# Optimization experiments

Hardware: AMD Instinct MI355X
Metric: run time of the kernel (lower is better)

Reference implementation:

```python
import jax, jax.numpy as jnp
import numpy as np

PC_RANGE = [-51.2, -51.2, -5.0, 51.2, 51.2, 3.0]
VOXEL = [0.1, 0.1, 0.2]
OSF = 8
NUM_PRIOR = 100
C = 256
BN_EPS = 1e-5
LN_EPS = 1e-5


def _conv(x, w, pad):
    # x: [B,C,H,W], w: [O,I,kh,kw]
    return jax.lax.conv_general_dilated(
        x, w, window_strides=(1, 1), padding=[(pad, pad), (pad, pad)],
        dimension_numbers=('NCHW', 'OIHW', 'NCHW'))


def _bn(x, g, b, m, v):
    scale = (g / jnp.sqrt(v + BN_EPS))[None, :, None, None]
    return (x - m[None, :, None, None]) * scale + b[None, :, None, None]


def setup_inputs() -> dict:
    key = jax.random.key(0)
    ks = jax.random.split(key, 24)
    s3 = 1.0 / np.sqrt(C * 9)
    s1 = 1.0 / np.sqrt(C)
    inp = {
        'bev_feat': jax.random.normal(ks[0], (4, C, 128, 128), jnp.float32),
        'template_anchor': jax.random.normal(ks[1], (4, 900, 11), jnp.float32),
        # shared_conv: 3x3 conv (no bias) + BN(eval) + ReLU
        'shared_w': jax.random.normal(ks[2], (C, C, 3, 3), jnp.float32) * s3,
        'bn1_g': jax.random.normal(ks[3], (C,), jnp.float32) * 0.1 + 1.0,
        'bn1_b': jax.random.normal(ks[4], (C,), jnp.float32) * 0.1,
        'bn1_m': jax.random.normal(ks[5], (C,), jnp.float32) * 0.1,
        'bn1_v': jax.random.uniform(ks[6], (C,), jnp.float32) + 0.5,
        # objectness: 3x3 conv (no bias) + BN + ReLU + 1x1 conv (bias=-2)
        'obj_w1': jax.random.normal(ks[7], (C, C, 3, 3), jnp.float32) * s3,
        'bn2_g': jax.random.normal(ks[8], (C,), jnp.float32) * 0.1 + 1.0,
        'bn2_b': jax.random.normal(ks[9], (C,), jnp.float32) * 0.1,
        'bn2_m': jax.random.normal(ks[10], (C,), jnp.float32) * 0.1,
        'bn2_v': jax.random.uniform(ks[11], (C,), jnp.float32) + 0.5,
        'obj_w2': jax.random.normal(ks[12], (1, C, 1, 1), jnp.float32) * s1,
        'obj_b2': jnp.full((1,), -2.0, jnp.float32),
        # feat_proj: Linear + LN + ReLU + Linear
        'fp_w1': jax.random.normal(ks[13], (C, C), jnp.float32) * s1,
        'fp_b1': jax.random.normal(ks[14], (C,), jnp.float32) * 0.01,
        'ln_g': jnp.ones((C,), jnp.float32),
        'ln_b': jnp.zeros((C,), jnp.float32),
        'fp_w2': jax.random.normal(ks[15], (C, C), jnp.float32) * s1,
        'fp_b2': jax.random.normal(ks[16], (C,), jnp.float32) * 0.01,
        # geometry heads (1x1 convs, bias init 0)
        'z_w': jax.random.normal(ks[17], (1, C, 1, 1), jnp.float32) * s1,
        'z_b': jnp.zeros((1,), jnp.float32),
        'dim_w': jax.random.normal(ks[18], (3, C, 1, 1), jnp.float32) * s1,
        'dim_b': jnp.zeros((3,), jnp.float32),
        'yaw_w': jax.random.normal(ks[19], (2, C, 1, 1), jnp.float32) * s1,
        'yaw_b': jnp.zeros((2,), jnp.float32),
        'vel_w': jax.random.normal(ks[20], (2, C, 1, 1), jnp.float32) * s1,
        'vel_b': jnp.zeros((2,), jnp.float32),
    }
    return inp


def _forward(bev_feat, template_anchor, shared_w, bn1_g, bn1_b, bn1_m, bn1_v,
             obj_w1, bn2_g, bn2_b, bn2_m, bn2_v, obj_w2, obj_b2,
             fp_w1, fp_b1, ln_g, ln_b, fp_w2, fp_b2,
             z_w, z_b, dim_w, dim_b, yaw_w, yaw_b, vel_w, vel_b):
    B, Cc, H, W = bev_feat.shape
    # shared_conv
    feat = jax.nn.relu(_bn(_conv(bev_feat, shared_w, 1), bn1_g, bn1_b, bn1_m, bn1_v))
    # objectness heatmap
    h = jax.nn.relu(_bn(_conv(feat, obj_w1, 1), bn2_g, bn2_b, bn2_m, bn2_v))
    heatmap = jax.nn.sigmoid(_conv(h, obj_w2, 0) + obj_b2[None, :, None, None])
    score = heatmap.reshape(B, H * W)
    K = min(NUM_PRIOR, H * W, template_anchor.shape[1])
    topk_score, topk_inds = jax.lax.top_k(score, K)  # [B,K]
    ys = topk_inds // W
    xs = topk_inds % W
    # gather BEV features at topk locations: [B,K,C]
    feat_flat = feat.reshape(B, Cc, H * W).transpose(0, 2, 1)
    gathered = jnp.take_along_axis(feat_flat, topk_inds[:, :, None], axis=1)
    # feat_proj: Linear + LN + ReLU + Linear
    x = gathered @ fp_w1.T + fp_b1
    mu = jnp.mean(x, axis=-1, keepdims=True)
    var = jnp.mean((x - mu) ** 2, axis=-1, keepdims=True)
    x = (x - mu) / jnp.sqrt(var + LN_EPS) * ln_g + ln_b
    x = jax.nn.relu(x)
    prior_feature = x @ fp_w2.T + fp_b2
    prior_feature = prior_feature * (1.0 + topk_score[:, :, None])
    # geometry heads (1x1 convs == linear on gathered features)
    z_pred = gathered @ z_w[:, :, 0, 0].T + z_b      # [B,K,1]
    dim_pred = gathered @ dim_w[:, :, 0, 0].T + dim_b  # [B,K,3]
    yaw_pred = gathered @ yaw_w[:, :, 0, 0].T + yaw_b  # [B,K,2]
    vel_pred = gathered @ vel_w[:, :, 0, 0].T + vel_b  # [B,K,2]
    # anchor update
    pa = template_anchor[:, :K, :]
    x_metric = (xs.astype(pa.dtype) + 0.5) * (VOXEL[0] * OSF) + PC_RANGE[0]
    y_metric = (ys.astype(pa.dtype) + 0.5) * (VOXEL[1] * OSF) + PC_RANGE[1]
    z_new = pa[..., 2] + 0.5 * z_pred[..., 0]
    dims_new = pa[..., 3:6] + 0.2 * jnp.clip(dim_pred, -1.0, 1.0)
    yaw = jnp.tanh(yaw_pred)
    nrm = jnp.maximum(jnp.sqrt(jnp.sum(yaw * yaw, axis=-1, keepdims=True)), 1e-6)
    yaw_new = 0.7 * pa[..., 6:8] + 0.3 * (yaw / nrm)
    vel_new = pa[..., 8:10] + 0.2 * jnp.clip(vel_pred, -2.0, 2.0)
    prior_anchor = jnp.concatenate([
        x_metric[..., None], y_metric[..., None], z_new[..., None],
        dims_new, yaw_new, vel_new, pa[..., 10:]], axis=-1)
    return prior_feature, prior_anchor, topk_score


def reference(bev_feat, template_anchor, shared_w, bn1_g, bn1_b, bn1_m, bn1_v,
              obj_w1, bn2_g, bn2_b, bn2_m, bn2_v, obj_w2, obj_b2,
              fp_w1, fp_b1, ln_g, ln_b, fp_w2, fp_b2,
              z_w, z_b, dim_w, dim_b, yaw_w, yaw_b, vel_w, vel_b):
    return _forward(bev_feat, template_anchor, shared_w, bn1_g, bn1_b, bn1_m, bn1_v,
                    obj_w1, bn2_g, bn2_b, bn2_m, bn2_v, obj_w2, obj_b2,
                    fp_w1, fp_b1, ln_g, ln_b, fp_w2, fp_b2,
                    z_w, z_b, dim_w, dim_b, yaw_w, yaw_b, vel_w, vel_b)
```

## Files before the change

### kernel.cpp

```cpp
#include <hip/hip_runtime.h>
#include <math.h>


typedef __attribute__((ext_vector_type(8))) short bf16x8;
typedef __attribute__((ext_vector_type(4))) float f32x4;

#define HW 16384
#define WPITCH 130
#define CCAP 192
#define PSTR 28
#define WSO_XN    0ULL
#define WSO_FEATB 34078720ULL
#define WSO_WP1   68157440ULL
#define WSO_WP2   69337088ULL
#define WSO_BNP   70516736ULL
#define WSO_LOG   70521856ULL
#define WSO_CAND  70784000ULL
#define WSO_CNT   70787072ULL
#define WSO_EXL   70787136ULL
#define WSO_TIDX  70790208ULL
#define WSO_TLOG  70791808ULL
#define WSO_W1N   70793408ULL
#define WSO_W2N   73152704ULL
#define WSO_A1P   WSO_XN
#define WSO_ACC2  28311552ULL

__device__ __forceinline__ float bf2f(short s) {
  return __uint_as_float(((unsigned)(unsigned short)s) << 16);
}
__device__ __forceinline__ short f2bf(float f) {
  unsigned u = __float_as_uint(f);
  u += 0x7fffu + ((u >> 16) & 1u);
  return (short)(u >> 16);
}
__device__ __forceinline__ void gll16(const void* g, void* l) {
  __builtin_amdgcn_global_load_lds(
      (const __attribute__((address_space(1))) void*)g,
      (__attribute__((address_space(3))) void*)l, 16, 0, 0);
}

__global__ void wprep2(const float* __restrict__ s1, const float* __restrict__ s2,
                       short* __restrict__ wp1, short* __restrict__ wp2,
                       float* __restrict__ wn1, float* __restrict__ wn2) {
  int bx = blockIdx.x;
  const float* src;
  short* wp;
  float* wn;
  if (bx >= 2304) {
    src = s2; wp = wp2; wn = wn2; bx -= 2304;
  } else {
    src = s1; wp = wp1; wn = wn1;
  }
  int i = bx * 256 + threadIdx.x;
  float v = src[i];
  int k = i % 9;
  int r = i / 9;
  int ci = r & 255;
  int co = r >> 8;
  wp[(k * 256 + co) * 256 + ci] = f2bf(v);
  wn[(ci * 9 + k) * 256 + co] = v;
}

__global__ void smallprep(const float* g1, const float* b1, const float* m1,
                          const float* v1, const float* g2, const float* b2,
                          const float* m2, const float* v2, const float* w2,
                          const float* ob2, float* __restrict__ bnp,
                          short* __restrict__ xn, short* __restrict__ featb,
                          float* __restrict__ logits) {
  const int blk = blockIdx.x, t = threadIdx.x;
  if (blk < 1024) {
    int i = blk * 256 + t;
    int c = i & 255;
    int r = i >> 8;
    int nh = r >> 1;
    int side = r & 1;
    size_t off = ((size_t)nh * WPITCH + (side ? 129 : 0)) * 256 + c;
    xn[off] = 0;
    featb[off] = 0;
  } else if (blk < 1280) {
    logits[(blk - 1024) * 256 + t] = ob2[0];
  } else {
    float s1 = g1[t] / sqrtf(v1[t] + 1e-5f);
    bnp[t] = s1;
    bnp[256 + t] = b1[t] - m1[t] * s1;
    float s2 = g2[t] / sqrtf(v2[t] + 1e-5f);
    bnp[512 + t] = s2;
    bnp[768 + t] = b2[t] - m2[t] * s2;
    bnp[1024 + t] = w2[t];
  }
}

__global__ __launch_bounds__(256) void nchw2nhwc(const float* __restrict__ in,
                                                 short* __restrict__ out) {
  __shared__ short tl[64 * 66];
  int n = blockIdx.z, c0 = blockIdx.y * 64, s0 = blockIdx.x * 64;
  int sl = threadIdx.x & 63, cl = threadIdx.x >> 6;
  for (int p = 0; p < 16; ++p) {
    int c = cl + p * 4;
    tl[c * 66 + sl] = f2bf(in[(((size_t)(n * 256 + c0 + c)) << 14) + s0 + sl]);
  }
  __syncthreads();
  int co = threadIdx.x & 63, so = threadIdx.x >> 6;
  for (int p = 0; p < 16; ++p) {
    int S = s0 + so + p * 4;
    int h = S >> 7, w = S & 127;
    out[(((size_t)(n * 128 + h)) * WPITCH + w + 1) * 256 + c0 + co] =
        tl[co * 66 + (so + p * 4)];
  }
}

template <int OUT_LOGITS>
__global__ __launch_bounds__(256) void conv3x3(const short* __restrict__ inp,
                                               const short* __restrict__ wp,
                                               const float* __restrict__ scale,
                                               const float* __restrict__ shift,
                                               const float* __restrict__ w2f,
                                               short* __restrict__ outb,
                                               float* __restrict__ logits) {
  __shared__ short a_sm[132 * 32];
  __shared__ short b_sm[3][128 * 32];
  const int t = threadIdx.x;
  const int wv = t >> 6, lane = t & 63;
  const int l15 = lane & 15, quad = lane >> 4;
  const int tile = blockIdx.x;
  const int img = tile >> 7;
  const int h = tile & 127;
  const int nblk = blockIdx.y;
  const int m0 = (wv & 1) << 6;
  const int n0 = (wv >> 1) << 6;

  f32x4 acc[4][4];
#pragma unroll
  for (int i = 0; i < 4; ++i)
#pragma unroll
    for (int j = 0; j < 4; ++j) {
      acc[i][j][0] = 0.f; acc[i][j][1] = 0.f;
      acc[i][j][2] = 0.f; acc[i][j][3] = 0.f;
    }

  for (int dhi = 0; dhi < 3; ++dhi) {
    const int hy = h + dhi - 1;
    if (hy < 0 || hy > 127) continue;
    const size_t arow = ((size_t)(img * 128 + hy)) * WPITCH;
    const short* wbase = wp + ((size_t)(dhi * 3 * 256 + nblk * 128)) * 256;

    for (int c0 = 0; c0 < 256; c0 += 32) {
      __syncthreads();
#pragma unroll
      for (int j = 0; j < 2; ++j) {
        const int seg = (j << 6) + (t >> 2);
        const int cc = t & 3;
        gll16(inp + (arow + seg) * 256 + c0 + cc * 8,
              a_sm + ((size_t)((j << 8) + t)) * 8);
      }
      if (t < 32) {
        const int r = t >> 4, dw = t & 15;
        const int* gsrc = (const int*)(inp + (arow + 128 + r) * 256 + c0) + dw;
        ((int*)a_sm)[(128 + r) * 16 + dw] = *gsrc;
      }
#pragma unroll
      for (int dwi = 0; dwi < 3; ++dwi) {
        const short* wtap = wbase + (size_t)dwi * 65536;
#pragma unroll
        for (int j = 0; j < 2; ++j) {
          const int nrow = (j << 6) + (t >> 2);
          const int cc = t & 3;
          gll16(wtap + (size_t)nrow * 256 + c0 + cc * 8,
                b_sm[dwi] + ((size_t)((j << 8) + t)) * 8);
        }
      }
      __syncthreads();

#pragma unroll
      for (int dwi = 0; dwi < 3; ++dwi) {
        bf16x8 af[4], bfr[4];
#pragma unroll
        for (int i = 0; i < 4; ++i)
          af[i] = *(const bf16x8*)(a_sm + (dwi + m0 + i * 16 + l15) * 32 + quad * 8);
#pragma unroll
        for (int i = 0; i < 4; ++i)
          bfr[i] = *(const bf16x8*)(b_sm[dwi] + (n0 + i * 16 + l15) * 32 + quad * 8);
#pragma unroll
        for (int i = 0; i < 4; ++i)
#pragma unroll
          for (int j = 0; j < 4; ++j)
            acc[i][j] = __builtin_amdgcn_mfma_f32_16x16x32_bf16(af[i], bfr[j],
                                                                acc[i][j], 0, 0, 0);
      }
    }
  }

  float sc[4], sh[4], wf[4];
#pragma unroll
  for (int j = 0; j < 4; ++j) {
    const int co = nblk * 128 + n0 + j * 16 + l15;
    sc[j] = scale[co];
    sh[j] = shift[co];
    if (OUT_LOGITS) wf[j] = w2f[co];
  }
  if (OUT_LOGITS) {
    float* lrow = logits + ((size_t)img << 14) + (h << 7);
#pragma unroll
    for (int i = 0; i < 4; ++i) {
#pragma unroll
      for (int r = 0; r < 4; ++r) {
        float part = 0.f;
#pragma unroll
        for (int j = 0; j < 4; ++j) {
          float v = fmaxf(acc[i][j][r] * sc[j] + sh[j], 0.f);
          part += v * wf[j];
        }
        part += __shfl_xor(part, 1);
        part += __shfl_xor(part, 2);
        part += __shfl_xor(part, 4);
        part += __shfl_xor(part, 8);
        if (l15 == 0)
          atomicAdd(&lrow[m0 + i * 16 + quad * 4 + r], part);
      }
    }
  } else {
    const size_t obase = ((size_t)(img * 128 + h)) * WPITCH + 1;
#pragma unroll
    for (int i = 0; i < 4; ++i) {
#pragma unroll
      for (int j = 0; j < 4; ++j) {
        const int co = nblk * 128 + n0 + j * 16 + l15;
#pragma unroll
        for (int r = 0; r < 4; ++r) {
          const int m = m0 + i * 16 + quad * 4 + r;
          float v = fmaxf(acc[i][j][r] * sc[j] + sh[j], 0.f);
          outb[(obase + m) * 256 + co] = f2bf(v);
        }
      }
    }
  }
}

__global__ __launch_bounds__(1024) void topk_radix(const float* __restrict__ logits,
                                                   int* __restrict__ cand,
                                                   int* __restrict__ cnt_out) {
  __shared__ int hist[2048];
  __shared__ int wsum[16];
  __shared__ unsigned sel_bin;
  __shared__ int sel_above;
  __shared__ int cntr;
  const int b = blockIdx.x, t = threadIdx.x;
  const int lane = t & 63, wid = t >> 6;
  const float* L = logits + (size_t)b * HW;
  const int base = t * 16;
  unsigned kv[16];
#pragma unroll
  for (int i = 0; i < 4; ++i) {
    float4 v = *(const float4*)(L + base + i * 4);
    float f4[4] = {v.x, v.y, v.z, v.w};
#pragma unroll
    for (int j = 0; j < 4; ++j) {
      unsigned u = __float_as_uint(f4[j]);
      kv[i * 4 + j] = u ^ (((unsigned)((int)u >> 31)) | 0x80000000u);
    }
  }
  unsigned prefix = 0, pmask = 0;
  int need = 128;
  const int shifts[3] = {21, 10, 0};
  const int nbs[3] = {2048, 2048, 1024};

  for (int lev = 0; lev < 3; ++lev) {
    const int shift = shifts[lev];
    const int nb = nbs[lev];
    hist[t] = 0;
    hist[t + 1024] = 0;
    __syncthreads();
#pragma unroll
    for (int i = 0; i < 16; ++i)
      if ((kv[i] & pmask) == prefix)
        atomicAdd(&hist[(kv[i] >> shift) & (nb - 1)], 1);
    __syncthreads();
    const int cs = nb >> 10;
    const int bin_hi = nb - 1 - t * cs;
    const int c_hi = hist[bin_hi];
    const int c_lo = (cs == 2) ? hist[bin_hi - 1] : 0;
    const int s = c_hi + c_lo;
    int inc = s;
    for (int off = 1; off < 64; off <<= 1) {
      int nbr = __shfl_up(inc, off);
      if (lane >= off) inc += nbr;
    }
    if (lane == 63) wsum[wid] = inc;
    __syncthreads();
    if (wid == 0) {
      int wv = (lane < 16) ? wsum[lane] : 0;
      for (int off = 1; off < 16; off <<= 1) {
        int nbr = __shfl_up(wv, off);
        if (lane >= off) wv += nbr;
      }
      if (lane < 16) wsum[lane] = wv;
    }
    __syncthreads();
    const int excl = inc - s + (wid ? wsum[wid - 1] : 0);
    if (excl < need && need <= excl + s) {
      if (need <= excl + c_hi) {
        sel_bin = (unsigned)bin_hi;
        sel_above = excl;
      } else {
        sel_bin = (unsigned)(bin_hi - 1);
        sel_above = excl + c_hi;
      }
    }
    __syncthreads();
    prefix |= sel_bin << shift;
    pmask |= ((unsigned)(nb - 1)) << shift;
    need -= sel_above;
    __syncthreads();
  }
  if (t == 0) cntr = 0;
  __syncthreads();
#pragma unroll
  for (int i = 0; i < 16; ++i) {
    if (kv[i] >= prefix) {
      int p = atomicAdd(&cntr, 1);
      if (p < CCAP) cand[b * CCAP + p] = base + i;
    }
  }
  __syncthreads();
  if (t == 0) cnt_out[b] = (cntr < CCAP) ? cntr : CCAP;
}

__device__ __forceinline__ void wload2(const float* __restrict__ wr,
                                       float w[2][9]) {
#pragma unroll
  for (int k = 0; k < 9; ++k) {
    w[0][k] = wr[k * 256];
    w[1][k] = wr[k * 256 + 128];
  }
}

__device__ __forceinline__ void conv_step2(const float* __restrict__ pc,
                                           const float w[2][9], float a[2][9]) {
  float xp[28];
  const float4* pr = (const float4*)pc;
#pragma unroll
  for (int q = 0; q < 7; ++q) {
    float4 v = pr[q];
    xp[q * 4 + 0] = v.x; xp[q * 4 + 1] = v.y;
    xp[q * 4 + 2] = v.z; xp[q * 4 + 3] = v.w;
  }
#pragma unroll
  for (int py = 0; py < 3; ++py)
#pragma unroll
    for (int px = 0; px < 3; ++px)
#pragma unroll
      for (int ky = 0; ky < 3; ++ky)
#pragma unroll
        for (int kx = 0; kx < 3; ++kx) {
          const float xv = xp[(py + ky) * 5 + px + kx];
          const int pp = py * 3 + px, kk = ky * 3 + kx;
          a[0][pp] += w[0][kk] * xv;
          a[1][pp] += w[1][kk] * xv;
        }
}

__global__ __launch_bounds__(128, 2) void rescore_a(
    const float* __restrict__ bev, const float* __restrict__ w1n,
    const int* __restrict__ cand, const int* __restrict__ cnt,
    float* __restrict__ a1part) {
  const int bx = blockIdx.x, b = blockIdx.y, z = blockIdx.z;
  const int t = threadIdx.x;
  const int n = cnt[b];
  const int c0 = bx * 2;
  if (c0 >= n) return;
  const int nc = (n - c0 < 2) ? (n - c0) : 2;
  const int ci0 = z << 6;
  __shared__ float patch[2 * 64 * PSTR];

  {
    const int TE = nc * 1600;
    int sg[2];
#pragma unroll
    for (int g = 0; g < 2; ++g) {
      int cc = c0 + g;
      sg[g] = cand[b * CCAP + ((cc < n) ? cc : (n - 1))];
    }
#pragma unroll
    for (int k = 0; k < 25; ++k) {
      int e = t + (k << 7);
      if (e < TE) {
        int g = (e >= 1600) ? 1 : 0;
        int rem = e - g * 1600;
        int ci = rem / 25;
        int rj = rem - ci * 25;
        int r = rj / 5;
        int j = rj - r * 5;
        int s = sg[g];
        int hy = (s >> 7) - 2 + r, wx = (s & 127) - 2 + j;
        float v = 0.f;
        if (hy >= 0 && hy < 128 && wx >= 0 && wx < 128)
          v = bev[(((size_t)(b * 256 + ci0 + ci)) << 14) + (hy << 7) + wx];
        patch[(g * 64 + ci) * PSTR + rj] = v;
      } else {
        int rem = e - 1600;
        int ci = rem / 25;
        int rj = rem - ci * 25;
        patch[(64 + ci) * PSTR + rj] = 0.f;
      }
    }
  }
  __syncthreads();

  const int col = t;
  float aA[2][9], aB[2][9];
#pragma unroll
  for (int h = 0; h < 2; ++h)
#pragma unroll
    for (int p = 0; p < 9; ++p) { aA[h][p] = 0.f; aB[h][p] = 0.f; }

  const float* p0 = patch;
  const float* p1 = patch + 64 * PSTR;
  const float* wbase = w1n + (size_t)ci0 * 2304 + col;

  float wA[2][9], wB[2][9];
  wload2(wbase, wA);
  for (int ci = 0; ci < 64; ci += 2) {
    wload2(wbase + (size_t)(ci + 1) * 2304, wB);
    conv_step2(p0 + ci * PSTR, wA, aA);
    conv_step2(p1 + ci * PSTR, wA, aB);
    if (ci + 2 < 64)
      wload2(wbase + (size_t)(ci + 2) * 2304, wA);
    conv_step2(p0 + (ci + 1) * PSTR, wB, aA);
    conv_step2(p1 + (ci + 1) * PSTR, wB, aB);
  }

#pragma unroll
  for (int g = 0; g < 2; ++g) {
    const int c = c0 + g;
    if (c < n) {
      const float (*a)[9] = g ? aB : aA;
      float* dst =
          a1part + ((((size_t)(b * CCAP + c) * 4 + z) * 9) << 8) + col;
#pragma unroll
      for (int p = 0; p < 9; ++p) {
        dst[p << 8] = a[0][p];
        dst[(p << 8) + 128] = a[1][p];
      }
    }
  }
}

__global__ __launch_bounds__(256) void rescore_b(const float* __restrict__ a1part,
                                                 const float* __restrict__ w2n,
                                                 const float* __restrict__ bnp,
                                                 const int* __restrict__ cnt,
                                                 float* __restrict__ acc2) {
  const int bx = blockIdx.x, b = blockIdx.y, z = blockIdx.z;
  const int t = threadIdx.x;
  const int n = cnt[b];
  const int cbase = bx * 8;
  if (cbase >= n) return;
  const int zb = z << 6;
  __shared__ float f9[8 * 64 * 12];

  const int cf = t & 63;
  const int pg = t >> 6;
  const int cfg = zb + cf;
  const float sc1 = bnp[cfg], sh1 = bnp[256 + cfg];
#pragma unroll
  for (int g = 0; g < 8; ++g) {
    const int c = cbase + g;
    if (c < n) {
      const float* src =
          a1part + ((((size_t)(b * CCAP + c)) * 36) << 8) + cfg;
      for (int p = pg; p < 9; p += 4) {
        float v = src[(size_t)(0 * 9 + p) << 8] + src[(size_t)(1 * 9 + p) << 8] +
                  src[(size_t)(2 * 9 + p) << 8] + src[(size_t)(3 * 9 + p) << 8];
        f9[(g * 64 + cf) * 12 + p] = fmaxf(v * sc1 + sh1, 0.f);
      }
    } else {
      for (int p = pg; p < 9; p += 4) f9[(g * 64 + cf) * 12 + p] = 0.f;
    }
  }
  __syncthreads();

  float acc[8];
#pragma unroll
  for (int g = 0; g < 8; ++g) acc[g] = 0.f;
  for (int ci = 0; ci < 64; ++ci) {
    const float* wr = w2n + (size_t)(zb + ci) * 2304 + t;
    float w9[9];
#pragma unroll
    for (int k = 0; k < 9; ++k) w9[k] = wr[k * 256];
#pragma unroll
    for (int g = 0; g < 8; ++g) {
      const float4* fp = (const float4*)(f9 + (g * 64 + ci) * 12);
      float4 f0 = fp[0], f1 = fp[1], f2 = fp[2];
      acc[g] += w9[0] * f0.x;
      acc[g] += w9[1] * f0.y;
      acc[g] += w9[2] * f0.z;
      acc[g] += w9[3] * f0.w;
      acc[g] += w9[4] * f1.x;
      acc[g] += w9[5] * f1.y;
      acc[g] += w9[6] * f1.z;
      acc[g] += w9[7] * f1.w;
      acc[g] += w9[8] * f2.x;
    }
  }
#pragma unroll
  for (int g = 0; g < 8; ++g) {
    const int c = cbase + g;
    if (c < n)
      acc2[((((size_t)(b * CCAP + c)) * 4 + z) << 8) + t] = acc[g];
  }
}

__global__ __launch_bounds__(256) void rescore_c(const float* __restrict__ acc2,
                                                 const float* __restrict__ bnp,
                                                 const float* __restrict__ b2,
                                                 const int* __restrict__ cnt,
                                                 float* __restrict__ exlog) {
  const int bx = blockIdx.x, b = blockIdx.y, t = threadIdx.x;
  const int lane = t & 63, wid = t >> 6;
  const int n = cnt[b];
  const int c = bx * 4 + wid;
  if (c >= n) return;
  const float* src = acc2 + (((size_t)(b * CCAP + c)) << 10);
  float p = 0.f;
#pragma unroll
  for (int j = 0; j < 4; ++j) {
    const int co = lane + j * 64;
    float v = ((src[co] + src[256 + co]) + src[512 + co]) + src[768 + co];
    p += fmaxf(v * bnp[512 + co] + bnp[768 + co], 0.f) * bnp[1024 + co];
  }
  for (int off = 32; off; off >>= 1) p += __shfl_xor(p, off);
  if (lane == 0) exlog[b * CCAP + c] = p + b2[0];
}

__global__ __launch_bounds__(CCAP) void final_topk(const float* __restrict__ exlog,
                                                   const int* __restrict__ cand,
                                                   const int* __restrict__ cnt,
                                                   int* __restrict__ tidx,
                                                   float* __restrict__ tlog) {
  const int b = blockIdx.x, t = threadIdx.x;
  __shared__ float v[CCAP];
  __shared__ int si[CCAP];
  const int n = cnt[b];
  float mv = (t < n) ? exlog[b * CCAP + t] : -3.0e38f;
  int s = (t < n) ? cand[b * CCAP + t] : 0x7FFFFFFF;
  v[t] = mv;
  si[t] = s;
  __syncthreads();
  int rank = 0;
  for (int j = 0; j < CCAP; ++j) {
    float vj = v[j];
    int sj = si[j];
    if (vj > mv || (vj == mv && sj < s)) ++rank;
  }
  if (t < n && rank < 100) {
    tidx[b * 100 + rank] = s;
    tlog[b * 100 + rank] = mv;
  }
}

__global__ __launch_bounds__(256) void head_kern(
    const short* __restrict__ featb, const int* __restrict__ tidx,
    const float* __restrict__ tlog, const float* __restrict__ tmpl,
    const float* __restrict__ w1, const float* __restrict__ b1,
    const float* __restrict__ lng, const float* __restrict__ lnb,
    const float* __restrict__ w2, const float* __restrict__ b2,
    const float* __restrict__ zw, const float* __restrict__ zb,
    const float* __restrict__ dmw, const float* __restrict__ dmb,
    const float* __restrict__ yw, const float* __restrict__ yb,
    const float* __restrict__ vw, const float* __restrict__ vb,
    float* __restrict__ out) {
  const int blk = blockIdx.x;
  const int b = blk / 100, q = blk % 100;
  const int t = threadIdx.x;
  const int lane = t & 63, wid = t >> 6;
  __shared__ float g[256];
  __shared__ float sx[256];
  __shared__ float red[4];
  __shared__ float heads[8];

  const int s = tidx[b * 100 + q];
  const float score = 1.f / (1.f + expf(-tlog[b * 100 + q]));
  const int ys = s >> 7, xs = s & 127;

  g[t] = bf2f(featb[(((size_t)(b * 128 + ys)) * WPITCH + xs + 1) * 256 + t]);
  __syncthreads();

  float x = b1[t];
  {
    const float* wr = w1 + (size_t)t * 256;
    for (int i = 0; i < 256; i += 4) {
      float4 wv = *(const float4*)(wr + i);
      x += g[i] * wv.x + g[i + 1] * wv.y + g[i + 2] * wv.z + g[i + 3] * wv.w;
    }
  }
  float sum = x;
  for (int off = 32; off; off >>= 1) sum += __shfl_xor(sum, off);
  if (lane == 0) red[wid] = sum;
  __syncthreads();
  float mu = (red[0] + red[1] + red[2] + red[3]) * (1.f / 256.f);
  __syncthreads();
  float d = x - mu;
  float q2 = d * d;
  for (int off = 32; off; off >>= 1) q2 += __shfl_xor(q2, off);
  if (lane == 0) red[wid] = q2;
  __syncthreads();
  float var = (red[0] + red[1] + red[2] + red[3]) * (1.f / 256.f);
  float xn = d * (1.f / sqrtf(var + 1e-5f)) * lng[t] + lnb[t];
  xn = fmaxf(xn, 0.f);
  sx[t] = xn;
  __syncthreads();
  float pf = b2[t];
  {
    const float* wr = w2 + (size_t)t * 256;
    for (int i = 0; i < 256; i += 4) {
      float4 wv = *(const float4*)(wr + i);
      pf += sx[i] * wv.x + sx[i + 1] * wv.y + sx[i + 2] * wv.z + sx[i + 3] * wv.w;
    }
  }
  pf *= (1.f + score);
  out[(size_t)(b * 100 + q) * 256 + t] = pf;

  const int k = t >> 5, l = t & 31;
  const float* hw;
  float hb;
  if (k == 0)      { hw = zw;                 hb = zb[0]; }
  else if (k < 4)  { hw = dmw + (k - 1) * 256; hb = dmb[k - 1]; }
  else if (k < 6)  { hw = yw + (k - 4) * 256;  hb = yb[k - 4]; }
  else             { hw = vw + (k - 6) * 256;  hb = vb[k - 6]; }
  float hp = 0.f;
#pragma unroll
  for (int r = 0; r < 8; ++r) {
    int i = l + r * 32;
    hp += g[i] * hw[i];
  }
  for (int off = 16; off; off >>= 1) hp += __shfl_xor(hp, off);
  if (l == 0) heads[k] = hp + hb;
  __syncthreads();

  if (t == 0) {
    const float* pa = tmpl + ((size_t)b * 900 + q) * 11;
    float p[11];
#pragma unroll
    for (int i = 0; i < 11; ++i) p[i] = pa[i];
    float a[11];
    a[0] = ((float)xs + 0.5f) * 0.8f - 51.2f;
    a[1] = ((float)ys + 0.5f) * 0.8f - 51.2f;
    a[2] = p[2] + 0.5f * heads[0];
#pragma unroll
    for (int i = 0; i < 3; ++i)
      a[3 + i] = p[3 + i] + 0.2f * fminf(fmaxf(heads[1 + i], -1.f), 1.f);
    float t0 = tanhf(heads[4]), t1 = tanhf(heads[5]);
    float nrm = fmaxf(sqrtf(t0 * t0 + t1 * t1), 1e-6f);
    a[6] = 0.7f * p[6] + 0.3f * t0 / nrm;
    a[7] = 0.7f * p[7] + 0.3f * t1 / nrm;
    a[8] = p[8] + 0.2f * fminf(fmaxf(heads[6], -2.f), 2.f);
    a[9] = p[9] + 0.2f * fminf(fmaxf(heads[7], -2.f), 2.f);
    a[10] = p[10];
    float* oa = out + 102400 + (size_t)(b * 100 + q) * 11;
#pragma unroll
    for (int i = 0; i < 11; ++i) oa[i] = a[i];
    out[106800 + b * 100 + q] = score;
  }
}

extern "C" void kernel_launch(void* const* d_in, const int* in_sizes, int n_in,
                              void* d_out, int out_size, void* d_ws, size_t ws_size,
                              hipStream_t stream) {
  (void)in_sizes; (void)n_in; (void)out_size; (void)ws_size;
  char* ws = (char*)d_ws;
  short* xn     = (short*)(ws + WSO_XN);
  short* featb  = (short*)(ws + WSO_FEATB);
  short* wp1    = (short*)(ws + WSO_WP1);
  short* wp2    = (short*)(ws + WSO_WP2);
  float* bnp    = (float*)(ws + WSO_BNP);
  float* logits = (float*)(ws + WSO_LOG);
  int*   cand   = (int*)(ws + WSO_CAND);
  int*   cnt    = (int*)(ws + WSO_CNT);
  float* exl    = (float*)(ws + WSO_EXL);
  int*   tidx   = (int*)(ws + WSO_TIDX);
  float* tlog   = (float*)(ws + WSO_TLOG);
  float* w1n    = (float*)(ws + WSO_W1N);
  float* w2n    = (float*)(ws + WSO_W2N);
  float* a1p    = (float*)(ws + WSO_A1P);
  float* acc2   = (float*)(ws + WSO_ACC2);

  const float* bev = (const float*)d_in[0];

  wprep2<<<4608, 256, 0, stream>>>((const float*)d_in[2], (const float*)d_in[7],
                                   wp1, wp2, w1n, w2n);
  smallprep<<<1281, 256, 0, stream>>>(
      (const float*)d_in[3], (const float*)d_in[4], (const float*)d_in[5],
      (const float*)d_in[6], (const float*)d_in[8], (const float*)d_in[9],
      (const float*)d_in[10], (const float*)d_in[11], (const float*)d_in[12],
      (const float*)d_in[13], bnp, xn, featb, logits);
  nchw2nhwc<<<dim3(256, 4, 4), 256, 0, stream>>>(bev, xn);
  conv3x3<0><<<dim3(512, 2), 256, 0, stream>>>(xn, wp1, bnp, bnp + 256,
                                               nullptr, featb, nullptr);
  conv3x3<1><<<dim3(512, 2), 256, 0, stream>>>(featb, wp2, bnp + 512, bnp + 768,
                                               bnp + 1024, nullptr, logits);
  topk_radix<<<4, 1024, 0, stream>>>(logits, cand, cnt);
  rescore_a<<<dim3(CCAP / 2, 4, 4), 128, 0, stream>>>(bev, w1n, cand, cnt, a1p);
  rescore_b<<<dim3(CCAP / 8, 4, 4), 256, 0, stream>>>(a1p, w2n, bnp, cnt, acc2);
  rescore_c<<<dim3(CCAP / 4, 4), 256, 0, stream>>>(acc2, bnp,
                                                   (const float*)d_in[13], cnt,
                                                   exl);
  final_topk<<<4, CCAP, 0, stream>>>(exl, cand, cnt, tidx, tlog);
  head_kern<<<400, 256, 0, stream>>>(
      featb, tidx, tlog, (const float*)d_in[1],
      (const float*)d_in[14], (const float*)d_in[15], (const float*)d_in[16],
      (const float*)d_in[17], (const float*)d_in[18], (const float*)d_in[19],
      (const float*)d_in[20], (const float*)d_in[21], (const float*)d_in[22],
      (const float*)d_in[23], (const float*)d_in[24], (const float*)d_in[25],
      (const float*)d_in[26], (const float*)d_in[27], (float*)d_out);
}
```

Before: 573.5 us.

## Restructure rescore_a to 4 candidates per block with output-channel halves

```diff
diff --git a/kernel.cpp b/kernel.cpp
--- a/kernel.cpp
+++ b/kernel.cpp
@@ -359,32 +359,33 @@
         }
 }
 
-__global__ __launch_bounds__(128, 2) void rescore_a(
+__global__ __launch_bounds__(256, 4) void rescore_a(
     const float* __restrict__ bev, const float* __restrict__ w1n,
     const int* __restrict__ cand, const int* __restrict__ cnt,
     float* __restrict__ a1part) {
   const int bx = blockIdx.x, b = blockIdx.y, z = blockIdx.z;
+  const int q = z >> 1, hf = z & 1;
   const int t = threadIdx.x;
   const int n = cnt[b];
-  const int c0 = bx * 2;
+  const int c0 = bx * 4;
   if (c0 >= n) return;
-  const int nc = (n - c0 < 2) ? (n - c0) : 2;
-  const int ci0 = z << 6;
-  __shared__ float patch[2 * 64 * PSTR];
+  const int nc = (n - c0 < 4) ? (n - c0) : 4;
+  const int ci0 = q << 6;
+  __shared__ float patch[4 * 64 * PSTR];
 
   {
     const int TE = nc * 1600;
-    int sg[2];
-#pragma unroll
-    for (int g = 0; g < 2; ++g) {
+    int sg[4];
+#pragma unroll
+    for (int g = 0; g < 4; ++g) {
       int cc = c0 + g;
       sg[g] = cand[b * CCAP + ((cc < n) ? cc : (n - 1))];
     }
 #pragma unroll
     for (int k = 0; k < 25; ++k) {
-      int e = t + (k << 7);
+      int e = t + (k << 8);
       if (e < TE) {
-        int g = (e >= 1600) ? 1 : 0;
+        int g = (e >= 3200) ? ((e >= 4800) ? 3 : 2) : ((e >= 1600) ? 1 : 0);
         int rem = e - g * 1600;
         int ci = rem / 25;
         int rj = rem - ci * 25;
@@ -397,50 +398,46 @@
           v = bev[(((size_t)(b * 256 + ci0 + ci)) << 14) + (hy << 7) + wx];
         patch[(g * 64 + ci) * PSTR + rj] = v;
       } else {
-        int rem = e - 1600;
+        int g2z = (e >= 3200) ? ((e >= 4800) ? 3 : 2) : 1;
+        int rem = e - g2z * 1600;
         int ci = rem / 25;
         int rj = rem - ci * 25;
-        patch[(64 + ci) * PSTR + rj] = 0.f;
-      }
-    }
-  }
-  __syncthreads();
-
-  const int col = t;
-  float aA[2][9], aB[2][9];
+        patch[(g2z * 64 + ci) * PSTR + rj] = 0.f;
+      }
+    }
+  }
+  __syncthreads();
+
+  const int col = t & 63;
+  const int g = t >> 6;
+  const int co0 = (hf << 6) + col;
+  float a[2][9];
 #pragma unroll
   for (int h = 0; h < 2; ++h)
 #pragma unroll
-    for (int p = 0; p < 9; ++p) { aA[h][p] = 0.f; aB[h][p] = 0.f; }
-
-  const float* p0 = patch;
-  const float* p1 = patch + 64 * PSTR;
-  const float* wbase = w1n + (size_t)ci0 * 2304 + col;
+    for (int p = 0; p < 9; ++p) a[h][p] = 0.f;
+
+  const float* pbase = patch + (g << 6) * PSTR;
+  const float* wbase = w1n + (size_t)ci0 * 2304 + co0;
 
   float wA[2][9], wB[2][9];
   wload2(wbase, wA);
   for (int ci = 0; ci < 64; ci += 2) {
     wload2(wbase + (size_t)(ci + 1) * 2304, wB);
-    conv_step2(p0 + ci * PSTR, wA, aA);
-    conv_step2(p1 + ci * PSTR, wA, aB);
+    conv_step2(pbase + ci * PSTR, wA, a);
     if (ci + 2 < 64)
       wload2(wbase + (size_t)(ci + 2) * 2304, wA);
-    conv_step2(p0 + (ci + 1) * PSTR, wB, aA);
-    conv_step2(p1 + (ci + 1) * PSTR, wB, aB);
-  }
-
-#pragma unroll
-  for (int g = 0; g < 2; ++g) {
+    conv_step2(pbase + (ci + 1) * PSTR, wB, a);
+  }
+
+  if (g < nc) {
     const int c = c0 + g;
-    if (c < n) {
-      const float (*a)[9] = g ? aB : aA;
-      float* dst =
-          a1part + ((((size_t)(b * CCAP + c) * 4 + z) * 9) << 8) + col;
-#pragma unroll
-      for (int p = 0; p < 9; ++p) {
-        dst[p << 8] = a[0][p];
-        dst[(p << 8) + 128] = a[1][p];
-      }
+    float* dst =
+        a1part + ((((size_t)(b * CCAP + c) * 4 + q) * 9) << 8) + co0;
+#pragma unroll
+    for (int p = 0; p < 9; ++p) {
+      dst[p << 8] = a[0][p];
+      dst[(p << 8) + 128] = a[1][p];
     }
   }
 }
@@ -699,7 +696,7 @@
   conv3x3<1><<<dim3(512, 2), 256, 0, stream>>>(featb, wp2, bnp + 512, bnp + 768,
                                                bnp + 1024, nullptr, logits);
   topk_radix<<<4, 1024, 0, stream>>>(logits, cand, cnt);
-  rescore_a<<<dim3(CCAP / 2, 4, 4), 128, 0, stream>>>(bev, w1n, cand, cnt, a1p);
+  rescore_a<<<dim3(CCAP / 4, 4, 8), 256, 0, stream>>>(bev, w1n, cand, cnt, a1p);
   rescore_b<<<dim3(CCAP / 8, 4, 4), 256, 0, stream>>>(a1p, w2n, bnp, cnt, acc2);
   rescore_c<<<dim3(CCAP / 4, 4), 256, 0, stream>>>(acc2, bnp,
                                                    (const float*)d_in[13], cnt,
```

After: 785.6 us. +37.0%, slower.
